# Kernel optimization log

Hardware: AMD Instinct MI355X
Metric: run time of the kernel (lower is better)

Reference implementation:

```python
import jax, jax.numpy as jnp
import numpy as np

B, C, H, W = 8, 256, 64, 64


def setup_inputs() -> dict:
    key = jax.random.key(0)
    ks = jax.random.split(key, 8)
    s = 1.0 / np.sqrt(C)
    return {
        "x": jax.random.normal(ks[0], (B, C, H, W), dtype=jnp.float32),
        "Wq": jax.random.normal(ks[1], (C, C), dtype=jnp.float32) * s,
        "bq": jax.random.normal(ks[2], (C,), dtype=jnp.float32) * 0.01,
        "Wk": jax.random.normal(ks[3], (C, C), dtype=jnp.float32) * s,
        "bk": jax.random.normal(ks[4], (C,), dtype=jnp.float32) * 0.01,
        "Wv": jax.random.normal(ks[5], (C, C), dtype=jnp.float32) * s,
        "bv": jax.random.normal(ks[6], (C,), dtype=jnp.float32) * 0.01,
        "gamma": jax.random.normal(ks[7], (1,), dtype=jnp.float32) * 0.1,
    }


def reference(x, Wq, bq, Wk, bk, Wv, bv, gamma):
    b, c, h, w = x.shape
    xf = x.reshape(b, c, h * w)                       # (B, C, N)
    # 1x1 conv == per-pixel linear: out_c = W @ in_c + bias
    q = jnp.einsum('oc,bcn->bon', Wq, xf) + bq[None, :, None]
    k = jnp.einsum('oc,bcn->bon', Wk, xf) + bk[None, :, None]
    v = jnp.einsum('oc,bcn->bon', Wv, xf) + bv[None, :, None]
    # attention_map[b, i, j] = sum_c q[b, c, i] * k[b, c, j]  (no scaling in original)
    scores = jnp.einsum('bci,bcj->bij', q, k)         # (B, N, N)
    attn = jax.nn.softmax(scores, axis=-1)
    # out[b, c, i] = sum_j v[b, c, j] * attn[b, i, j]
    out = jnp.einsum('bcj,bij->bci', v, attn)
    out = out.reshape(b, c, h, w)
    return x + gamma[0] * out
```

## Files before the change

### kernel.cpp

```cpp
#include <hip/hip_runtime.h>

#define BATCH 8
#define CCH 256
#define NPOS 4096
#define LOG2E 1.4426950408889634f

typedef __bf16 bf16x8 __attribute__((ext_vector_type(8)));
typedef float f32x4 __attribute__((ext_vector_type(4)));
typedef int i32x4 __attribute__((ext_vector_type(4)));

typedef const __attribute__((address_space(1))) void GAS;
typedef __attribute__((address_space(3))) void LAS;

#define CFENCE() __asm__ volatile("" ::: "memory")
#define WAIT_VM8()  do { CFENCE(); __builtin_amdgcn_s_waitcnt(0x0F78); CFENCE(); } while (0)
#define WAIT_LGKM0() do { CFENCE(); __builtin_amdgcn_s_waitcnt(0xC07F); CFENCE(); } while (0)
#define BAR_RAW() do { CFENCE(); __builtin_amdgcn_s_barrier(); CFENCE(); } while (0)

__device__ __forceinline__ unsigned short f2bf(float f) {
  unsigned u = __builtin_bit_cast(unsigned, f);
  u += 0x7fffu + ((u >> 16) & 1u);
  return (unsigned short)(u >> 16);
}

__device__ __forceinline__ bf16x8 ld_bf8(const unsigned short* p) {
  i32x4 t = *reinterpret_cast<const i32x4*>(p);
  return __builtin_bit_cast(bf16x8, t);
}

template<int CTRL>
__device__ __forceinline__ float dpp_rorf(float x) {
  return __builtin_bit_cast(float,
      __builtin_amdgcn_update_dpp(0, __builtin_bit_cast(int, x), CTRL, 0xF, 0xF, false));
}

__device__ __forceinline__ float fexp2(float x) {
#if __has_builtin(__builtin_amdgcn_exp2f)
  return __builtin_amdgcn_exp2f(x);
#else
  return __expf(x * 0.6931471805599453f);
#endif
}

__global__ void cvt_kernel(const float* __restrict__ Wq,
                           const float* __restrict__ Wk,
                           const float* __restrict__ Wv,
                           unsigned short* __restrict__ dst)
{
  const int idx = blockIdx.x * 256 + threadIdx.x;
  const float* src = (idx < 65536) ? Wq : ((idx < 131072) ? Wk : Wv);
  dst[idx] = f2bf(src[idx & 65535]);
}

__global__ __launch_bounds__(256, 3)
void qkv_kernel(const float* __restrict__ x,
                const unsigned short* __restrict__ Wall,
                const float* __restrict__ bq,
                const float* __restrict__ bk,
                const float* __restrict__ bv,
                unsigned short* __restrict__ qT,
                unsigned short* __restrict__ kT,
                unsigned short* __restrict__ vG)
{
  __shared__ __align__(16) unsigned short xT[64 * 264];
  __shared__ __align__(16) unsigned short tbuf[64 * 72];

  const int b   = blockIdx.x;
  const int i0  = blockIdx.y * 64;
  const int tid = threadIdx.x;
  const int w   = tid >> 6;
  const int l   = tid & 63;
  const int n   = l & 15;
  const int q4  = l >> 4;

  {
    const int li = tid & 15;
    const int cg = tid >> 4;
#pragma unroll
    for (int it = 0; it < 16; ++it) {
      const int c = it * 16 + cg;
      f32x4 f = *reinterpret_cast<const f32x4*>(x + ((size_t)b * CCH + c) * NPOS + i0 + li * 4);
#pragma unroll
      for (int e = 0; e < 4; ++e) xT[(li * 4 + e) * 264 + c] = f2bf(f[e]);
    }
  }
  __syncthreads();

  const size_t qbase = (size_t)b * NPOS * CCH;
  bool first = true;

  for (int s = 0; s < 3; ++s) {
    const float* bias = (s == 0) ? bq : (s == 1) ? bk : bv;
    for (int op = 0; op < 4; ++op) {
      const int obase = op * 64;

      const unsigned short* Wp = Wall + s * 65536 + (size_t)(obase + w * 16 + n) * CCH + q4 * 8;
      bf16x8 wfr[8];
#pragma unroll
      for (int kk = 0; kk < 8; ++kk) wfr[kk] = ld_bf8(Wp + kk * 32);

      float bo[4];
#pragma unroll
      for (int r = 0; r < 4; ++r) bo[r] = bias[obase + w * 16 + q4 * 4 + r];

      f32x4 acc[4];
#pragma unroll
      for (int pt = 0; pt < 4; ++pt) {
        acc[pt] = {0.f, 0.f, 0.f, 0.f};
#pragma unroll
        for (int kk = 0; kk < 8; ++kk) {
          bf16x8 bfr = ld_bf8(&xT[(pt * 16 + n) * 264 + kk * 32 + q4 * 8]);
          acc[pt] = __builtin_amdgcn_mfma_f32_16x16x32_bf16(wfr[kk], bfr, acc[pt], 0, 0, 0);
        }
      }

      if (!first) __syncthreads();
      first = false;
      if (s < 2) {
        const float sc = (s == 0) ? LOG2E : 1.0f;
#pragma unroll
        for (int pt = 0; pt < 4; ++pt)
#pragma unroll
          for (int r = 0; r < 4; ++r)
            tbuf[(pt * 16 + n) * 72 + w * 16 + q4 * 4 + r] = f2bf((acc[pt][r] + bo[r]) * sc);
      } else {
#pragma unroll
        for (int pt = 0; pt < 4; ++pt)
#pragma unroll
          for (int r = 0; r < 4; ++r)
            tbuf[(w * 16 + q4 * 4 + r) * 72 + pt * 16 + n] = f2bf(acc[pt][r] + bo[r]);
      }
      __syncthreads();

      if (s < 2) {
        unsigned short* dst = (s == 0 ? qT : kT) + qbase;
#pragma unroll
        for (int it2 = 0; it2 < 2; ++it2) {
          const int idx = it2 * 256 + tid;
          const int pos = idx >> 3, ow = (idx & 7) * 8;
          i32x4 d = *reinterpret_cast<const i32x4*>(&tbuf[pos * 72 + ow]);
          *reinterpret_cast<i32x4*>(&dst[(size_t)(i0 + pos) * CCH + obase + ow]) = d;
        }
      } else {
#pragma unroll
        for (int it2 = 0; it2 < 2; ++it2) {
          const int idx = it2 * 256 + tid;
          const int o = idx >> 3, pw = (idx & 7) * 8;
          i32x4 d = *reinterpret_cast<const i32x4*>(&tbuf[o * 72 + pw]);
          *reinterpret_cast<i32x4*>(&vG[qbase + (size_t)(obase + o) * NPOS + i0 + pw]) = d;
        }
      }
    }
  }
}

__global__ __launch_bounds__(256, 2)
void attn_kernel(const unsigned short* __restrict__ qT,
                 const unsigned short* __restrict__ kT,
                 const unsigned short* __restrict__ vG,
                 const float* __restrict__ x,
                 const float* __restrict__ gamma,
                 float* __restrict__ out)
{
  __shared__ __align__(16) unsigned short kbuf[2][64 * 256];
  __shared__ __align__(16) unsigned short pbuf[64 * 64];
  __shared__ float stat_lds[64];

  const int b   = blockIdx.x;
  const int i0  = blockIdx.y * 64;
  const int tid = threadIdx.x;
  const int w   = tid >> 6;
  const int l   = tid & 63;
  const int n   = l & 15;
  const int q4  = l >> 4;
  const int nsw = n & 7;

  const unsigned short* qTb = qT + (size_t)b * NPOS * CCH;
  const unsigned short* kTb = kT + (size_t)b * NPOS * CCH;
  const unsigned short* vb  = vG + (size_t)b * NPOS * CCH;

  bf16x8 afr[8];
  {
    const unsigned short* qrow = qTb + (size_t)(i0 + w * 16 + n) * CCH + q4 * 8;
#pragma unroll
    for (int kk = 0; kk < 8; ++kk)
      afr[kk] = ld_bf8(qrow + kk * 32);
  }

  {
#pragma unroll
    for (int it = 0; it < 8; ++it) {
      const int t = w * 8 + it;
      const int j = 2 * t + (l >> 5);
      const int gp = l & 31;
      const int g  = gp ^ (j & 7);
      const unsigned short* src = kTb + (size_t)j * CCH + g * 8;
      unsigned short* dst = &kbuf[0][t * 512];
      __builtin_amdgcn_global_load_lds((GAS*)src, (LAS*)dst, 16, 0, 0);
    }
  }

  f32x4 O[16];
#pragma unroll
  for (int t = 0; t < 16; ++t) O[t] = {0.f, 0.f, 0.f, 0.f};
  float mrow[4] = {-1e30f, -1e30f, -1e30f, -1e30f};
  float lrow[4] = {0.f, 0.f, 0.f, 0.f};

  for (int jt = 0; jt < 64; ++jt) {
    const int j0 = jt * 64;
    const unsigned short* kb = kbuf[jt & 1];

    i32x4 vreg[8];
#pragma unroll
    for (int ct = 0; ct < 4; ++ct) {
      const unsigned short* vp = vb + (size_t)(w * 64 + ct * 16 + n) * NPOS + j0 + q4 * 8;
      vreg[ct * 2]     = *reinterpret_cast<const i32x4*>(vp);
      vreg[ct * 2 + 1] = *reinterpret_cast<const i32x4*>(vp + 32);
    }

    WAIT_VM8();
    BAR_RAW();

    f32x4 sacc[4];
#pragma unroll
    for (int nt = 0; nt < 4; ++nt) {
      const unsigned short* krow = kb + (nt * 16 + n) * 256;
      sacc[nt] = {0.f, 0.f, 0.f, 0.f};
#pragma unroll
      for (int kk = 0; kk < 8; ++kk) {
        const int gp = (kk * 4 + q4) ^ nsw;
        bf16x8 bfr = ld_bf8(krow + gp * 8);
        sacc[nt] = __builtin_amdgcn_mfma_f32_16x16x32_bf16(afr[kk], bfr, sacc[nt], 0, 0, 0);
      }
    }

    float a_r[4];
#pragma unroll
    for (int r = 0; r < 4; ++r) {
      float tm = fmaxf(fmaxf(sacc[0][r], sacc[1][r]), fmaxf(sacc[2][r], sacc[3][r]));
      tm = fmaxf(tm, dpp_rorf<0x121>(tm));
      tm = fmaxf(tm, dpp_rorf<0x122>(tm));
      tm = fmaxf(tm, dpp_rorf<0x124>(tm));
      tm = fmaxf(tm, dpp_rorf<0x128>(tm));
      const float mnew = fmaxf(mrow[r], tm);
      a_r[r] = fexp2(mrow[r] - mnew);
      float s = 0.f;
#pragma unroll
      for (int nt = 0; nt < 4; ++nt) {
        const float p = fexp2(sacc[nt][r] - mnew);
        sacc[nt][r] = p;
        s += p;
      }
      s += dpp_rorf<0x121>(s);
      s += dpp_rorf<0x122>(s);
      s += dpp_rorf<0x124>(s);
      s += dpp_rorf<0x128>(s);
      lrow[r] = lrow[r] * a_r[r] + s;
      mrow[r] = mnew;
    }

    if (n == 0) {
#pragma unroll
      for (int r = 0; r < 4; ++r) stat_lds[w * 16 + q4 * 4 + r] = a_r[r];
    }
#pragma unroll
    for (int r = 0; r < 4; ++r) {
      const int row = w * 16 + q4 * 4 + r;
      const int rs  = row & 7;
#pragma unroll
      for (int nt = 0; nt < 4; ++nt) {
        const int g = nt * 2 + (n >> 3);
        pbuf[row * 64 + ((g ^ rs) << 3) + (n & 7)] = f2bf(sacc[nt][r]);
      }
    }

    {
      const int j0n = ((jt + 1) & 63) * 64;
      unsigned short* bufn = kbuf[(jt + 1) & 1];
#pragma unroll
      for (int it = 0; it < 8; ++it) {
        const int t = w * 8 + it;
        const int j = 2 * t + (l >> 5);
        const int gp = l & 31;
        const int g  = gp ^ (j & 7);
        const unsigned short* src = kTb + (size_t)(j0n + j) * CCH + g * 8;
        unsigned short* dst = &bufn[t * 512];
        __builtin_amdgcn_global_load_lds((GAS*)src, (LAS*)dst, 16, 0, 0);
      }
    }

    WAIT_LGKM0();
    BAR_RAW();

#pragma unroll
    for (int it = 0; it < 4; ++it) {
      const float al = stat_lds[it * 16 + n];
#pragma unroll
      for (int ct = 0; ct < 4; ++ct) {
        f32x4& o = O[ct * 4 + it];
        o[0] *= al; o[1] *= al; o[2] *= al; o[3] *= al;
      }
    }

    bf16x8 pf[8];
#pragma unroll
    for (int it = 0; it < 4; ++it) {
      const int rowb = (it * 16 + n) * 64;
      pf[it * 2 + 0] = ld_bf8(&pbuf[rowb + ((q4 ^ nsw) << 3)]);
      pf[it * 2 + 1] = ld_bf8(&pbuf[rowb + (((4 + q4) ^ nsw) << 3)]);
    }
#pragma unroll
    for (int ct = 0; ct < 4; ++ct) {
      bf16x8 vf0 = __builtin_bit_cast(bf16x8, vreg[ct * 2]);
      bf16x8 vf1 = __builtin_bit_cast(bf16x8, vreg[ct * 2 + 1]);
#pragma unroll
      for (int it = 0; it < 4; ++it) {
        O[ct * 4 + it] = __builtin_amdgcn_mfma_f32_16x16x32_bf16(vf0, pf[it * 2 + 0], O[ct * 4 + it], 0, 0, 0);
        O[ct * 4 + it] = __builtin_amdgcn_mfma_f32_16x16x32_bf16(vf1, pf[it * 2 + 1], O[ct * 4 + it], 0, 0, 0);
      }
    }
  }

  __syncthreads();
  if (n == 0) {
#pragma unroll
    for (int r = 0; r < 4; ++r) stat_lds[w * 16 + q4 * 4 + r] = lrow[r];
  }
  __syncthreads();

  const float g = gamma[0];
#pragma unroll
  for (int it = 0; it < 4; ++it) {
    const float sc = g / stat_lds[it * 16 + n];
    const int ipos = i0 + it * 16 + n;
#pragma unroll
    for (int ct = 0; ct < 4; ++ct) {
#pragma unroll
      for (int r = 0; r < 4; ++r) {
        const int c = w * 64 + ct * 16 + q4 * 4 + r;
        const size_t idx = ((size_t)(b * CCH + c)) * NPOS + ipos;
        out[idx] = x[idx] + sc * O[ct * 4 + it][r];
      }
    }
  }
}

extern "C" void kernel_launch(void* const* d_in, const int* in_sizes, int n_in,
                              void* d_out, int out_size, void* d_ws, size_t ws_size,
                              hipStream_t stream)
{
  const float* x     = (const float*)d_in[0];
  const float* Wq    = (const float*)d_in[1];
  const float* bq    = (const float*)d_in[2];
  const float* Wk    = (const float*)d_in[3];
  const float* bk    = (const float*)d_in[4];
  const float* Wv    = (const float*)d_in[5];
  const float* bv    = (const float*)d_in[6];
  const float* gamma = (const float*)d_in[7];
  float* out = (float*)d_out;

  unsigned short* ws   = (unsigned short*)d_ws;
  unsigned short* Wall = ws;
  unsigned short* qT   = ws + 196608;
  unsigned short* kT   = qT + (size_t)BATCH * NPOS * CCH;
  unsigned short* vG   = kT + (size_t)BATCH * NPOS * CCH;

  cvt_kernel<<<768, 256, 0, stream>>>(Wq, Wk, Wv, Wall);
  qkv_kernel<<<dim3(8, 64), 256, 0, stream>>>(x, Wall, bq, bk, bv, qT, kT, vG);
  attn_kernel<<<dim3(8, 64), 256, 0, stream>>>(qT, kT, vG, x, gamma, out);
}
```

Measured before the change: 314.4 us.

## Restructure attention kernel around 32x32 MFMA with lazy softmax rescaling

Rewrites the attention main loop so each wave computes a 32x32 score tile with 32x32x16 bf16 MFMAs. Waves are split into i-halves and j-halves, and each pair exchanges bf16 P fragments and row statistics through LDS. Row max and sum reductions use v_permlane32_swap instead of DPP chains, and bf16 packing uses v_cvt_pk_bf16_f32. The online softmax now starts from a fixed reference max and rescales O only when some lane's max grows by more than 8. This removes most per-tile exp and multiply work and the P round-trip through a swizzled buffer. The price is a reliance on the expected score range and heavier register use for the 16-wide accumulators and V prefetch.

```diff
diff --git a/kernel.cpp b/kernel.cpp
--- a/kernel.cpp
+++ b/kernel.cpp
@@ -7,13 +7,14 @@
 
 typedef __bf16 bf16x8 __attribute__((ext_vector_type(8)));
 typedef float f32x4 __attribute__((ext_vector_type(4)));
+typedef float f32x16 __attribute__((ext_vector_type(16)));
 typedef int i32x4 __attribute__((ext_vector_type(4)));
 
 typedef const __attribute__((address_space(1))) void GAS;
 typedef __attribute__((address_space(3))) void LAS;
 
 #define CFENCE() __asm__ volatile("" ::: "memory")
-#define WAIT_VM8()  do { CFENCE(); __builtin_amdgcn_s_waitcnt(0x0F78); CFENCE(); } while (0)
+#define WAIT_VM0()   do { CFENCE(); __builtin_amdgcn_s_waitcnt(0x0F70); CFENCE(); } while (0)
 #define WAIT_LGKM0() do { CFENCE(); __builtin_amdgcn_s_waitcnt(0xC07F); CFENCE(); } while (0)
 #define BAR_RAW() do { CFENCE(); __builtin_amdgcn_s_barrier(); CFENCE(); } while (0)
 
@@ -28,19 +29,34 @@
   return __builtin_bit_cast(bf16x8, t);
 }
 
-template<int CTRL>
-__device__ __forceinline__ float dpp_rorf(float x) {
-  return __builtin_bit_cast(float,
-      __builtin_amdgcn_update_dpp(0, __builtin_bit_cast(int, x), CTRL, 0xF, 0xF, false));
-}
-
 __device__ __forceinline__ float fexp2(float x) {
 #if __has_builtin(__builtin_amdgcn_exp2f)
   return __builtin_amdgcn_exp2f(x);
 #else
-  return __expf(x * 0.6931471805599453f);
+  return __builtin_exp2f(x);
 #endif
 }
+
+__device__ __forceinline__ unsigned cvtpk(float lo, float hi) {
+  unsigned r;
+  asm("v_cvt_pk_bf16_f32 %0, %1, %2" : "=v"(r) : "v"(lo), "v"(hi));
+  return r;
+}
+__device__ __forceinline__ void plswap(unsigned& a, unsigned& b) {
+  asm("v_permlane32_swap_b32 %0, %1" : "+v"(a), "+v"(b));
+}
+__device__ __forceinline__ float xmax32(float v) {
+  unsigned a = __builtin_bit_cast(unsigned, v), b = a;
+  plswap(a, b);
+  return fmaxf(__builtin_bit_cast(float, a), __builtin_bit_cast(float, b));
+}
+__device__ __forceinline__ float xadd32(float v) {
+  unsigned a = __builtin_bit_cast(unsigned, v), b = a;
+  plswap(a, b);
+  return __builtin_bit_cast(float, a) + __builtin_bit_cast(float, b);
+}
+
+template <int N> struct IC { static constexpr int v = N; };
 
 __global__ void cvt_kernel(const float* __restrict__ Wq,
                            const float* __restrict__ Wk,
@@ -145,9 +161,9 @@
 #pragma unroll
         for (int it2 = 0; it2 < 2; ++it2) {
           const int idx = it2 * 256 + tid;
-          const int o = idx >> 3, pw = (idx & 7) * 8;
-          i32x4 d = *reinterpret_cast<const i32x4*>(&tbuf[o * 72 + pw]);
-          *reinterpret_cast<i32x4*>(&vG[qbase + (size_t)(obase + o) * NPOS + i0 + pw]) = d;
+          const int o = idx >> 3, pw2 = (idx & 7) * 8;
+          i32x4 d = *reinterpret_cast<const i32x4*>(&tbuf[o * 72 + pw2]);
+          *reinterpret_cast<i32x4*>(&vG[qbase + (size_t)(obase + o) * NPOS + i0 + pw2]) = d;
         }
       }
     }
@@ -163,128 +179,136 @@
                  float* __restrict__ out)
 {
   __shared__ __align__(16) unsigned short kbuf[2][64 * 256];
-  __shared__ __align__(16) unsigned short pbuf[64 * 64];
-  __shared__ float stat_lds[64];
+  __shared__ __align__(16) unsigned pfrag[4][64][8];
+  __shared__ __align__(8)  float stats[4][32][2];
 
   const int b   = blockIdx.x;
   const int i0  = blockIdx.y * 64;
   const int tid = threadIdx.x;
   const int w   = tid >> 6;
   const int l   = tid & 63;
-  const int n   = l & 15;
-  const int q4  = l >> 4;
-  const int nsw = n & 7;
+  const int l31 = l & 31;
+  const int g0  = l >> 5;
+  const int ih  = w >> 1;
+  const int jh  = w & 1;
+  const int pw  = w ^ 1;
 
   const unsigned short* qTb = qT + (size_t)b * NPOS * CCH;
   const unsigned short* kTb = kT + (size_t)b * NPOS * CCH;
   const unsigned short* vb  = vG + (size_t)b * NPOS * CCH;
 
-  bf16x8 afr[8];
+  bf16x8 qf[16];
   {
-    const unsigned short* qrow = qTb + (size_t)(i0 + w * 16 + n) * CCH + q4 * 8;
-#pragma unroll
-    for (int kk = 0; kk < 8; ++kk)
-      afr[kk] = ld_bf8(qrow + kk * 32);
-  }
-
-  {
-#pragma unroll
-    for (int it = 0; it < 8; ++it) {
-      const int t = w * 8 + it;
-      const int j = 2 * t + (l >> 5);
-      const int gp = l & 31;
-      const int g  = gp ^ (j & 7);
-      const unsigned short* src = kTb + (size_t)j * CCH + g * 8;
-      unsigned short* dst = &kbuf[0][t * 512];
-      __builtin_amdgcn_global_load_lds((GAS*)src, (LAS*)dst, 16, 0, 0);
-    }
-  }
-
-  f32x4 O[16];
-#pragma unroll
-  for (int t = 0; t < 16; ++t) O[t] = {0.f, 0.f, 0.f, 0.f};
-  float mrow[4] = {-1e30f, -1e30f, -1e30f, -1e30f};
-  float lrow[4] = {0.f, 0.f, 0.f, 0.f};
-
-  for (int jt = 0; jt < 64; ++jt) {
-    const int j0 = jt * 64;
-    const unsigned short* kb = kbuf[jt & 1];
-
-    i32x4 vreg[8];
+    const unsigned short* qrow = qTb + (size_t)(i0 + ih * 32 + l31) * CCH + g0 * 8;
+#pragma unroll
+    for (int kt = 0; kt < 16; ++kt) qf[kt] = ld_bf8(qrow + kt * 16);
+  }
+
+  unsigned kaddr[4];
+#pragma unroll
+  for (int q = 0; q < 4; ++q)
+    kaddr[q] = (unsigned)((jh * 32 + l31) * 512 + (((g0 + 2 * q) ^ (l & 7)) << 4));
+
+  unsigned kdoff[8];
+#pragma unroll
+  for (int it = 0; it < 8; ++it) {
+    const int j  = 2 * (w * 8 + it) + g0;
+    const int gg = l31 ^ (j & 7);
+    kdoff[it] = (unsigned)(j * (CCH * 2) + gg * 16);
+  }
+
+  unsigned voff[4];
+#pragma unroll
+  for (int ct = 0; ct < 4; ++ct)
+    voff[ct] = (unsigned)(((jh * 128 + ct * 32 + l31) * NPOS + g0 * 8) * 2);
+  const unsigned kcho0 = (unsigned)(jh * 64);
+  const unsigned kcho1 = (unsigned)((jh ^ 1) * 64);
+
+#pragma unroll
+  for (int it = 0; it < 8; ++it) {
+    const unsigned short* src = (const unsigned short*)((const char*)kTb + kdoff[it]);
+    unsigned short* dst = &kbuf[0][(w * 8 + it) * 512];
+    __builtin_amdgcn_global_load_lds((GAS*)src, (LAS*)dst, 16, 0, 0);
+  }
+
+  f32x16 O[4];
+#pragma unroll
+  for (int ct = 0; ct < 4; ++ct)
+#pragma unroll
+    for (int r = 0; r < 16; ++r) O[ct][r] = 0.f;
+  float mcur = 64.f;
+  float lrow = 0.f;
+
+  auto step = [&](int jt, auto BUFTAG) {
+    constexpr int BUF = decltype(BUFTAG)::v;
+
+    WAIT_VM0();
+    BAR_RAW();
+
+    f32x16 sacc;
+#pragma unroll
+    for (int r = 0; r < 16; ++r) sacc[r] = 0.f;
+#pragma unroll
+    for (int kt = 0; kt < 16; ++kt) {
+      const unsigned short* kp = (const unsigned short*)(
+          (const char*)(&kbuf[BUF][0]) + kaddr[kt & 3] + (kt >> 2) * 128);
+      sacc = __builtin_amdgcn_mfma_f32_32x32x16_bf16(ld_bf8(kp), qf[kt], sacc, 0, 0, 0);
+    }
+
+    float mw;
+    {
+      float a0 = fmaxf(sacc[0], sacc[1]),   a1 = fmaxf(sacc[2], sacc[3]);
+      float a2 = fmaxf(sacc[4], sacc[5]),   a3 = fmaxf(sacc[6], sacc[7]);
+      float a4 = fmaxf(sacc[8], sacc[9]),   a5 = fmaxf(sacc[10], sacc[11]);
+      float a6 = fmaxf(sacc[12], sacc[13]), a7 = fmaxf(sacc[14], sacc[15]);
+      a0 = fmaxf(a0, a1); a2 = fmaxf(a2, a3); a4 = fmaxf(a4, a5); a6 = fmaxf(a6, a7);
+      mw = xmax32(fmaxf(fmaxf(a0, a2), fmaxf(a4, a6)));
+    }
+
+    float p_[16];
+#pragma unroll
+    for (int r = 0; r < 16; ++r) p_[r] = fexp2(sacc[r] - mcur);
+
+    float sw;
+    {
+      float s0 = (p_[0] + p_[1]) + (p_[2] + p_[3]);
+      float s1 = (p_[4] + p_[5]) + (p_[6] + p_[7]);
+      float s2 = (p_[8] + p_[9]) + (p_[10] + p_[11]);
+      float s3 = (p_[12] + p_[13]) + (p_[14] + p_[15]);
+      sw = xadd32((s0 + s1) + (s2 + s3));
+    }
+
+    i32x4 vreg[16];
 #pragma unroll
     for (int ct = 0; ct < 4; ++ct) {
-      const unsigned short* vp = vb + (size_t)(w * 64 + ct * 16 + n) * NPOS + j0 + q4 * 8;
-      vreg[ct * 2]     = *reinterpret_cast<const i32x4*>(vp);
-      vreg[ct * 2 + 1] = *reinterpret_cast<const i32x4*>(vp + 32);
-    }
-
-    WAIT_VM8();
-    BAR_RAW();
-
-    f32x4 sacc[4];
-#pragma unroll
-    for (int nt = 0; nt < 4; ++nt) {
-      const unsigned short* krow = kb + (nt * 16 + n) * 256;
-      sacc[nt] = {0.f, 0.f, 0.f, 0.f};
-#pragma unroll
-      for (int kk = 0; kk < 8; ++kk) {
-        const int gp = (kk * 4 + q4) ^ nsw;
-        bf16x8 bfr = ld_bf8(krow + gp * 8);
-        sacc[nt] = __builtin_amdgcn_mfma_f32_16x16x32_bf16(afr[kk], bfr, sacc[nt], 0, 0, 0);
-      }
-    }
-
-    float a_r[4];
-#pragma unroll
-    for (int r = 0; r < 4; ++r) {
-      float tm = fmaxf(fmaxf(sacc[0][r], sacc[1][r]), fmaxf(sacc[2][r], sacc[3][r]));
-      tm = fmaxf(tm, dpp_rorf<0x121>(tm));
-      tm = fmaxf(tm, dpp_rorf<0x122>(tm));
-      tm = fmaxf(tm, dpp_rorf<0x124>(tm));
-      tm = fmaxf(tm, dpp_rorf<0x128>(tm));
-      const float mnew = fmaxf(mrow[r], tm);
-      a_r[r] = fexp2(mrow[r] - mnew);
-      float s = 0.f;
-#pragma unroll
-      for (int nt = 0; nt < 4; ++nt) {
-        const float p = fexp2(sacc[nt][r] - mnew);
-        sacc[nt][r] = p;
-        s += p;
-      }
-      s += dpp_rorf<0x121>(s);
-      s += dpp_rorf<0x122>(s);
-      s += dpp_rorf<0x124>(s);
-      s += dpp_rorf<0x128>(s);
-      lrow[r] = lrow[r] * a_r[r] + s;
-      mrow[r] = mnew;
-    }
-
-    if (n == 0) {
-#pragma unroll
-      for (int r = 0; r < 4; ++r) stat_lds[w * 16 + q4 * 4 + r] = a_r[r];
-    }
-#pragma unroll
-    for (int r = 0; r < 4; ++r) {
-      const int row = w * 16 + q4 * 4 + r;
-      const int rs  = row & 7;
-#pragma unroll
-      for (int nt = 0; nt < 4; ++nt) {
-        const int g = nt * 2 + (n >> 3);
-        pbuf[row * 64 + ((g ^ rs) << 3) + (n & 7)] = f2bf(sacc[nt][r]);
-      }
-    }
+      const char* vbase = (const char*)vb + voff[ct];
+      vreg[ct * 4 + 0] = *(const i32x4*)(vbase + kcho0);
+      vreg[ct * 4 + 1] = *(const i32x4*)(vbase + kcho0 + 32);
+      vreg[ct * 4 + 2] = *(const i32x4*)(vbase + kcho1);
+      vreg[ct * 4 + 3] = *(const i32x4*)(vbase + kcho1 + 32);
+    }
+
+    unsigned U0 = cvtpk(p_[0], p_[1]),   U1 = cvtpk(p_[2], p_[3]);
+    unsigned U2 = cvtpk(p_[4], p_[5]),   U3 = cvtpk(p_[6], p_[7]);
+    unsigned U4 = cvtpk(p_[8], p_[9]),   U5 = cvtpk(p_[10], p_[11]);
+    unsigned U6 = cvtpk(p_[12], p_[13]), U7 = cvtpk(p_[14], p_[15]);
+    unsigned s0a = U0, s0b = U2; plswap(s0a, s0b);
+    unsigned s1a = U1, s1b = U3; plswap(s1a, s1b);
+    unsigned s2a = U4, s2b = U6; plswap(s2a, s2b);
+    unsigned s3a = U5, s3b = U7; plswap(s3a, s3b);
+    i32x4 ownA = { (int)s0a, (int)s1a, (int)s0b, (int)s1b };
+    i32x4 ownB = { (int)s2a, (int)s3a, (int)s2b, (int)s3b };
+    *(i32x4*)&pfrag[w][l][0] = ownA;
+    *(i32x4*)&pfrag[w][l][4] = ownB;
+    if (!g0) { stats[w][l31][0] = mw; stats[w][l31][1] = sw; }
 
     {
-      const int j0n = ((jt + 1) & 63) * 64;
-      unsigned short* bufn = kbuf[(jt + 1) & 1];
+      const unsigned koffn = (unsigned)(((jt + 1) & 63) * 32768);
 #pragma unroll
       for (int it = 0; it < 8; ++it) {
-        const int t = w * 8 + it;
-        const int j = 2 * t + (l >> 5);
-        const int gp = l & 31;
-        const int g  = gp ^ (j & 7);
-        const unsigned short* src = kTb + (size_t)(j0n + j) * CCH + g * 8;
-        unsigned short* dst = &bufn[t * 512];
+        const unsigned short* src =
+            (const unsigned short*)((const char*)kTb + (kdoff[it] + koffn));
+        unsigned short* dst = &kbuf[BUF ^ 1][(w * 8 + it) * 512];
         __builtin_amdgcn_global_load_lds((GAS*)src, (LAS*)dst, 16, 0, 0);
       }
     }
@@ -292,55 +316,59 @@
     WAIT_LGKM0();
     BAR_RAW();
 
-#pragma unroll
-    for (int it = 0; it < 4; ++it) {
-      const float al = stat_lds[it * 16 + n];
-#pragma unroll
-      for (int ct = 0; ct < 4; ++ct) {
-        f32x4& o = O[ct * 4 + it];
-        o[0] *= al; o[1] *= al; o[2] *= al; o[3] *= al;
-      }
-    }
-
-    bf16x8 pf[8];
-#pragma unroll
-    for (int it = 0; it < 4; ++it) {
-      const int rowb = (it * 16 + n) * 64;
-      pf[it * 2 + 0] = ld_bf8(&pbuf[rowb + ((q4 ^ nsw) << 3)]);
-      pf[it * 2 + 1] = ld_bf8(&pbuf[rowb + (((4 + q4) ^ nsw) << 3)]);
-    }
+    i32x4 oppA = *(const i32x4*)&pfrag[pw][l][0];
+    i32x4 oppB = *(const i32x4*)&pfrag[pw][l][4];
+    const float mp = stats[pw][l31][0];
+    const float sp = stats[pw][l31][1];
+
+    const bf16x8 FB0 = __builtin_bit_cast(bf16x8, ownA);
+    const bf16x8 FB1 = __builtin_bit_cast(bf16x8, ownB);
+    const bf16x8 FB2 = __builtin_bit_cast(bf16x8, oppA);
+    const bf16x8 FB3 = __builtin_bit_cast(bf16x8, oppB);
 #pragma unroll
     for (int ct = 0; ct < 4; ++ct) {
-      bf16x8 vf0 = __builtin_bit_cast(bf16x8, vreg[ct * 2]);
-      bf16x8 vf1 = __builtin_bit_cast(bf16x8, vreg[ct * 2 + 1]);
-#pragma unroll
-      for (int it = 0; it < 4; ++it) {
-        O[ct * 4 + it] = __builtin_amdgcn_mfma_f32_16x16x32_bf16(vf0, pf[it * 2 + 0], O[ct * 4 + it], 0, 0, 0);
-        O[ct * 4 + it] = __builtin_amdgcn_mfma_f32_16x16x32_bf16(vf1, pf[it * 2 + 1], O[ct * 4 + it], 0, 0, 0);
-      }
-    }
-  }
-
-  __syncthreads();
-  if (n == 0) {
-#pragma unroll
-    for (int r = 0; r < 4; ++r) stat_lds[w * 16 + q4 * 4 + r] = lrow[r];
-  }
-  __syncthreads();
-
-  const float g = gamma[0];
-#pragma unroll
-  for (int it = 0; it < 4; ++it) {
-    const float sc = g / stat_lds[it * 16 + n];
-    const int ipos = i0 + it * 16 + n;
-#pragma unroll
-    for (int ct = 0; ct < 4; ++ct) {
-#pragma unroll
-      for (int r = 0; r < 4; ++r) {
-        const int c = w * 64 + ct * 16 + q4 * 4 + r;
-        const size_t idx = ((size_t)(b * CCH + c)) * NPOS + ipos;
-        out[idx] = x[idx] + sc * O[ct * 4 + it][r];
-      }
+      O[ct] = __builtin_amdgcn_mfma_f32_32x32x16_bf16(
+          __builtin_bit_cast(bf16x8, vreg[ct * 4 + 0]), FB0, O[ct], 0, 0, 0);
+      O[ct] = __builtin_amdgcn_mfma_f32_32x32x16_bf16(
+          __builtin_bit_cast(bf16x8, vreg[ct * 4 + 1]), FB1, O[ct], 0, 0, 0);
+      O[ct] = __builtin_amdgcn_mfma_f32_32x32x16_bf16(
+          __builtin_bit_cast(bf16x8, vreg[ct * 4 + 2]), FB2, O[ct], 0, 0, 0);
+      O[ct] = __builtin_amdgcn_mfma_f32_32x32x16_bf16(
+          __builtin_bit_cast(bf16x8, vreg[ct * 4 + 3]), FB3, O[ct], 0, 0, 0);
+    }
+
+    const float mt = fmaxf(mw, mp);
+    lrow += sw + sp;
+    const int upd = mt > mcur + 8.f;
+    if (__any(upd)) {
+      const float mn = upd ? mt : mcur;
+      const float al = fexp2(mcur - mn);
+      mcur = mn;
+      lrow *= al;
+#pragma unroll
+      for (int ct = 0; ct < 4; ++ct)
+#pragma unroll
+        for (int r = 0; r < 16; ++r) O[ct][r] *= al;
+    }
+
+#pragma unroll
+    for (int ct = 0; ct < 4; ++ct) voff[ct] += 128;
+  };
+
+  for (int jt2 = 0; jt2 < 32; ++jt2) {
+    step(2 * jt2,     IC<0>{});
+    step(2 * jt2 + 1, IC<1>{});
+  }
+
+  const float sc = gamma[0] / lrow;
+  const int ipos = i0 + ih * 32 + l31;
+#pragma unroll
+  for (int ct = 0; ct < 4; ++ct) {
+#pragma unroll
+    for (int r = 0; r < 16; ++r) {
+      const int c = jh * 128 + ct * 32 + (r & 3) + 8 * (r >> 2) + 4 * g0;
+      const size_t idx = ((size_t)(b * CCH + c)) * NPOS + ipos;
+      out[idx] = x[idx] + sc * O[ct][r];
     }
   }
 }
```

Result: slower. 523.9 us (+66.6%).

## Transpose QK^T MFMA output so each lane owns one query row

Applied to the files above, without the earlier changes.

Swaps the MFMA operand order for the score computation so each lane holds four consecutive key columns of a single query row. Per-row max and sum now need only intra-lane reductions plus two cross-lane shuffles, replacing four rows of DPP reductions. One running max and sum per lane replaces four. The P tile is packed with v_cvt_pk_bf16_f32 and written to LDS as 8-byte stores instead of scalar 2-byte stores. The risk is that __shfl_xor goes through LDS permute (ds_bpermute) and can be slower than DPP, and the new swizzled pbuf layout must match the reads.

```diff
diff --git a/kernel.cpp b/kernel.cpp
--- a/kernel.cpp
+++ b/kernel.cpp
@@ -8,6 +8,7 @@
 typedef __bf16 bf16x8 __attribute__((ext_vector_type(8)));
 typedef float f32x4 __attribute__((ext_vector_type(4)));
 typedef int i32x4 __attribute__((ext_vector_type(4)));
+typedef int i32x2 __attribute__((ext_vector_type(2)));
 
 typedef const __attribute__((address_space(1))) void GAS;
 typedef __attribute__((address_space(3))) void LAS;
@@ -28,18 +29,18 @@
   return __builtin_bit_cast(bf16x8, t);
 }
 
-template<int CTRL>
-__device__ __forceinline__ float dpp_rorf(float x) {
-  return __builtin_bit_cast(float,
-      __builtin_amdgcn_update_dpp(0, __builtin_bit_cast(int, x), CTRL, 0xF, 0xF, false));
-}
-
 __device__ __forceinline__ float fexp2(float x) {
 #if __has_builtin(__builtin_amdgcn_exp2f)
   return __builtin_amdgcn_exp2f(x);
 #else
-  return __expf(x * 0.6931471805599453f);
+  return __builtin_exp2f(x);
 #endif
+}
+
+__device__ __forceinline__ unsigned cvtpk(float lo, float hi) {
+  unsigned r;
+  asm("v_cvt_pk_bf16_f32 %0, %1, %2" : "=v"(r) : "v"(lo), "v"(hi));
+  return r;
 }
 
 __global__ void cvt_kernel(const float* __restrict__ Wq,
@@ -145,9 +146,9 @@
 #pragma unroll
         for (int it2 = 0; it2 < 2; ++it2) {
           const int idx = it2 * 256 + tid;
-          const int o = idx >> 3, pw = (idx & 7) * 8;
-          i32x4 d = *reinterpret_cast<const i32x4*>(&tbuf[o * 72 + pw]);
-          *reinterpret_cast<i32x4*>(&vG[qbase + (size_t)(obase + o) * NPOS + i0 + pw]) = d;
+          const int o = idx >> 3, pw2 = (idx & 7) * 8;
+          i32x4 d = *reinterpret_cast<const i32x4*>(&tbuf[o * 72 + pw2]);
+          *reinterpret_cast<i32x4*>(&vG[qbase + (size_t)(obase + o) * NPOS + i0 + pw2]) = d;
         }
       }
     }
@@ -203,8 +204,8 @@
   f32x4 O[16];
 #pragma unroll
   for (int t = 0; t < 16; ++t) O[t] = {0.f, 0.f, 0.f, 0.f};
-  float mrow[4] = {-1e30f, -1e30f, -1e30f, -1e30f};
-  float lrow[4] = {0.f, 0.f, 0.f, 0.f};
+  float mrow = -1e30f;
+  float lrow = 0.f;
 
   for (int jt = 0; jt < 64; ++jt) {
     const int j0 = jt * 64;
@@ -230,47 +231,48 @@
       for (int kk = 0; kk < 8; ++kk) {
         const int gp = (kk * 4 + q4) ^ nsw;
         bf16x8 bfr = ld_bf8(krow + gp * 8);
-        sacc[nt] = __builtin_amdgcn_mfma_f32_16x16x32_bf16(afr[kk], bfr, sacc[nt], 0, 0, 0);
-      }
-    }
-
-    float a_r[4];
-#pragma unroll
-    for (int r = 0; r < 4; ++r) {
-      float tm = fmaxf(fmaxf(sacc[0][r], sacc[1][r]), fmaxf(sacc[2][r], sacc[3][r]));
-      tm = fmaxf(tm, dpp_rorf<0x121>(tm));
-      tm = fmaxf(tm, dpp_rorf<0x122>(tm));
-      tm = fmaxf(tm, dpp_rorf<0x124>(tm));
-      tm = fmaxf(tm, dpp_rorf<0x128>(tm));
-      const float mnew = fmaxf(mrow[r], tm);
-      a_r[r] = fexp2(mrow[r] - mnew);
-      float s = 0.f;
-#pragma unroll
-      for (int nt = 0; nt < 4; ++nt) {
+        sacc[nt] = __builtin_amdgcn_mfma_f32_16x16x32_bf16(bfr, afr[kk], sacc[nt], 0, 0, 0);
+      }
+    }
+
+    float tm;
+    {
+      float a0 = fmaxf(fmaxf(sacc[0][0], sacc[0][1]), fmaxf(sacc[0][2], sacc[0][3]));
+      float a1 = fmaxf(fmaxf(sacc[1][0], sacc[1][1]), fmaxf(sacc[1][2], sacc[1][3]));
+      float a2 = fmaxf(fmaxf(sacc[2][0], sacc[2][1]), fmaxf(sacc[2][2], sacc[2][3]));
+      float a3 = fmaxf(fmaxf(sacc[3][0], sacc[3][1]), fmaxf(sacc[3][2], sacc[3][3]));
+      tm = fmaxf(fmaxf(a0, a1), fmaxf(a2, a3));
+      tm = fmaxf(tm, __shfl_xor(tm, 16));
+      tm = fmaxf(tm, __shfl_xor(tm, 32));
+    }
+    const float mnew = fmaxf(mrow, tm);
+    const float alpha = fexp2(mrow - mnew);
+    float s = 0.f;
+#pragma unroll
+    for (int nt = 0; nt < 4; ++nt) {
+#pragma unroll
+      for (int r = 0; r < 4; ++r) {
         const float p = fexp2(sacc[nt][r] - mnew);
         sacc[nt][r] = p;
         s += p;
       }
-      s += dpp_rorf<0x121>(s);
-      s += dpp_rorf<0x122>(s);
-      s += dpp_rorf<0x124>(s);
-      s += dpp_rorf<0x128>(s);
-      lrow[r] = lrow[r] * a_r[r] + s;
-      mrow[r] = mnew;
-    }
-
-    if (n == 0) {
-#pragma unroll
-      for (int r = 0; r < 4; ++r) stat_lds[w * 16 + q4 * 4 + r] = a_r[r];
-    }
-#pragma unroll
-    for (int r = 0; r < 4; ++r) {
-      const int row = w * 16 + q4 * 4 + r;
-      const int rs  = row & 7;
+    }
+    s += __shfl_xor(s, 16);
+    s += __shfl_xor(s, 32);
+    lrow = lrow * alpha + s;
+    mrow = mnew;
+
+    if (q4 == 0) stat_lds[w * 16 + n] = alpha;
+
+    {
+      const int rowb = (w * 16 + n) * 64;
 #pragma unroll
       for (int nt = 0; nt < 4; ++nt) {
-        const int g = nt * 2 + (n >> 3);
-        pbuf[row * 64 + ((g ^ rs) << 3) + (n & 7)] = f2bf(sacc[nt][r]);
+        const unsigned lo = cvtpk(sacc[nt][0], sacc[nt][1]);
+        const unsigned hi = cvtpk(sacc[nt][2], sacc[nt][3]);
+        const int pg = (2 * nt + (q4 >> 1)) ^ nsw;
+        i32x2 dv = { (int)lo, (int)hi };
+        *reinterpret_cast<i32x2*>(&pbuf[rowb + pg * 8 + (q4 & 1) * 4]) = dv;
       }
     }
 
@@ -322,10 +324,7 @@
   }
 
   __syncthreads();
-  if (n == 0) {
-#pragma unroll
-    for (int r = 0; r < 4; ++r) stat_lds[w * 16 + q4 * 4 + r] = lrow[r];
-  }
+  if (q4 == 0) stat_lds[w * 16 + n] = lrow;
   __syncthreads();
 
   const float g = gamma[0];
```

New measurement: 301.5 us. 4.1% less time.
